# Kernel optimization log

Measured on AMD Instinct MI355X. Metric: run time of the kernel, lower is better.

## Reference

```python
import jax, jax.numpy as jnp
import numpy as np

B, L, D, DIN, S, R, K = 2, 1024, 1024, 2048, 16, 64, 4


def setup_inputs() -> dict:
    key = jax.random.key(0)
    ks = jax.random.split(key, 8)
    f = lambda k, sh, sc: jax.random.normal(k, sh, jnp.float32) * sc
    return {
        "x": f(ks[0], (B, L, D), 1.0),
        "norm_w": jnp.ones((D,), jnp.float32),
        "W_in": f(ks[1], (D, 2 * DIN), D ** -0.5),
        "conv_w": f(ks[2], (DIN, 1, K), 0.5),
        "conv_b": jnp.zeros((DIN,), jnp.float32),
        "W_x": f(ks[3], (DIN, R + 2 * S), DIN ** -0.5),
        "W_dt": f(ks[4], (R, DIN), R ** -0.5),
        "b_dt": f(ks[5], (DIN,), 0.1),
        "A_log": jnp.log(jnp.broadcast_to(jnp.arange(1, S + 1, dtype=jnp.float32), (DIN, S))),
        "D_skip": jnp.ones((DIN,), jnp.float32),
        "W_out": f(ks[6], (DIN, D), DIN ** -0.5),
    }


def reference(x, norm_w, W_in, conv_w, conv_b, W_x, W_dt, b_dt, A_log, D_skip, W_out):
    eps = 1e-5
    # RMSNorm
    xn = x * jax.lax.rsqrt(jnp.mean(x * x, axis=-1, keepdims=True) + eps) * norm_w
    # input projection -> (x_branch, gate)
    xz = xn @ W_in                       # [B,L,2*DIN]
    xi, z = jnp.split(xz, 2, axis=-1)
    # causal depthwise conv1d along L
    xt = jnp.transpose(xi, (0, 2, 1))    # [B,DIN,L]
    xc = jax.lax.conv_general_dilated(xt, conv_w, (1,), [(K - 1, 0)],
                                      feature_group_count=DIN)
    xc = jnp.transpose(xc, (0, 2, 1)) + conv_b
    xc = jax.nn.silu(xc)                 # [B,L,DIN]
    # input-dependent SSM parameters
    xd = xc @ W_x                        # [B,L,R+2S]
    dt, Bm, Cm = jnp.split(xd, [R, R + S], axis=-1)
    dt = jax.nn.softplus(dt @ W_dt + b_dt)           # [B,L,DIN]
    A = -jnp.exp(A_log)                              # [DIN,S]
    dA = jnp.exp(dt[..., None] * A)                  # [B,L,DIN,S]
    dBu = (dt * xc)[..., None] * Bm[:, :, None, :]   # [B,L,DIN,S]
    # selective scan: h_t = dA_t * h_{t-1} + dBu_t (parallel associative scan)
    def comb(c1, c2):
        a1, b1 = c1
        a2, b2 = c2
        return a1 * a2, a2 * b1 + b2
    _, h = jax.lax.associative_scan(comb, (dA, dBu), axis=1)
    y = jnp.einsum('blds,bls->bld', h, Cm) + D_skip * xc
    y = y * jax.nn.silu(z)
    return x + y @ W_out
```

## Files before the change

### kernel.cpp

```cpp
#include <hip/hip_runtime.h>

#define B_    2
#define L_    1024
#define D_    1024
#define DIN_  2048
#define S_    16
#define R_    64
#define NTOK  (B_ * L_)
#define NCH   32
#define LC    (L_ / NCH)

typedef unsigned short u16;
typedef short bf16x8 __attribute__((ext_vector_type(8)));
typedef float f32x4  __attribute__((ext_vector_type(4)));

__device__ __forceinline__ u16 f2bf(float f) {
    union { float f; unsigned u; } v; v.f = f;
    return (u16)((v.u + 0x7FFFu + ((v.u >> 16) & 1u)) >> 16);
}
__device__ __forceinline__ float bf2f(u16 b) {
    union { unsigned u; float f; } v; v.u = (unsigned)b << 16;
    return v.f;
}

__device__ __forceinline__ void transp_tile(
    const float* __restrict__ src, u16* __restrict__ dst,
    int R, int Csrc, int cx, int cy, int tx, int ty) {
    __shared__ float tile[32][33];
    int c0 = cx * 32, r0 = cy * 32;
#pragma unroll
    for (int i = 0; i < 32; i += 8)
        tile[ty + i][tx] = (c0 + tx < Csrc)
            ? src[(size_t)(r0 + ty + i) * Csrc + c0 + tx] : 0.f;
    __syncthreads();
#pragma unroll
    for (int i = 0; i < 32; i += 8)
        dst[(size_t)(c0 + ty + i) * R + r0 + tx] = f2bf(tile[tx][ty + i]);
}

__global__ __launch_bounds__(256) void prep_kernel(
    const float* __restrict__ x, const float* __restrict__ nw, u16* __restrict__ xn,
    const float* __restrict__ W_in,  u16* __restrict__ WinT,
    const float* __restrict__ W_out, u16* __restrict__ WoutT,
    const float* __restrict__ W_x,   u16* __restrict__ WxT,
    const float* __restrict__ W_dt,  u16* __restrict__ WdtT) {
    int bid = blockIdx.x;
    if (bid < NTOK) {
        int row = bid;
        const float4 v = ((const float4*)(x + (size_t)row * D_))[threadIdx.x];
        float ss = v.x * v.x + v.y * v.y + v.z * v.z + v.w * v.w;
#pragma unroll
        for (int o = 32; o > 0; o >>= 1) ss += __shfl_down(ss, o);
        __shared__ float red[4];
        if ((threadIdx.x & 63) == 0) red[threadIdx.x >> 6] = ss;
        __syncthreads();
        float tot = red[0] + red[1] + red[2] + red[3];
        float sc = rsqrtf(tot * (1.f / (float)D_) + 1e-5f);
        const float4 wv = ((const float4*)nw)[threadIdx.x];
        ushort4 o;
        o.x = f2bf(v.x * sc * wv.x);
        o.y = f2bf(v.y * sc * wv.y);
        o.z = f2bf(v.z * sc * wv.z);
        o.w = f2bf(v.w * sc * wv.w);
        ((ushort4*)(xn + (size_t)row * D_))[threadIdx.x] = o;
        return;
    }
    int b2 = bid - NTOK;
    int tx = threadIdx.x & 31, ty = threadIdx.x >> 5;
    if (b2 < 4096) {
        transp_tile(W_in, WinT, D_, 2 * DIN_, b2 % 128, b2 / 128, tx, ty);
    } else if (b2 < 6144) {
        int b = b2 - 4096;
        transp_tile(W_out, WoutT, DIN_, D_, b % 32, b / 32, tx, ty);
    } else if (b2 < 6400) {
        int b = b2 - 6144;
        transp_tile(W_x, WxT, DIN_, 96, b % 4, b / 4, tx, ty);
    } else {
        int b = b2 - 6400;
        transp_tile(W_dt, WdtT, R_, DIN_, b % 64, b / 64, tx, ty);
    }
}

#define BK 32
template<int BM, int BN, int CX>
__global__ __launch_bounds__(512, 8) void gemm_bf16(
    const u16* __restrict__ A, int lda,
    const u16* __restrict__ Bt, int ldb,
    float* __restrict__ C, u16* __restrict__ Cbf, int ldc,
    const float* __restrict__ aux,
    int M, int N, int K, int mode) {
    constexpr int WROWS = BM / 32;
    constexpr int WCOLS = BN / 32;
    static_assert(WROWS * WCOLS == 8, "8 waves");
    constexpr int FM = 2;
    constexpr int FN = 2;
    constexpr int ABYTES = BM * BK * 2;
    constexpr int BBYTES = BN * BK * 2;
    __shared__ __align__(16) u16 As[2][BM * BK];
    __shared__ __align__(16) u16 Bs[2][BN * BK];
    const int t = threadIdx.x;
    const int w = t >> 6;
    const int l = t & 63;
    const int lr = l & 15;
    const int kg = l >> 4;
    const int wm = (w / WCOLS) * 32;
    const int wn = (w % WCOLS) * 32;

    const int GX = gridDim.x, GY = gridDim.y;
    int h = blockIdx.x + GX * (blockIdx.y + GY * blockIdx.z);
    int xcd = h & 7, pos = h >> 3;
    int ncx = GX / CX;
    int chunk = (GX * GY * gridDim.z) >> 3;
    int rpc = chunk / CX;
    int bx = (xcd % ncx) * CX + pos % CX;
    int r  = (xcd / ncx) * rpc + pos / CX;
    int by = r % GY;
    int bz = r / GY;

    const int row0 = by * BM;
    const int col0 = bx * BN;
    const int kbase = bz * K;

    auto stage = [&](int buf, int k0) {
        if (t < ABYTES / 16) {
            int off = t * 16;
            int grow = off >> 6;
            int sw = ((off >> 4) & 3) ^ ((grow >> 1) & 3);
            const u16* ga = A + (size_t)(row0 + grow) * lda + k0 + sw * 8;
            __builtin_amdgcn_global_load_lds(
                (const __attribute__((address_space(1))) unsigned int*)(const void*)ga,
                (__attribute__((address_space(3))) unsigned int*)(void*)&As[buf][off >> 1],
                16, 0, 0);
        }
        if (t < BBYTES / 16) {
            int off = t * 16;
            int grow = off >> 6;
            int sw = ((off >> 4) & 3) ^ ((grow >> 1) & 3);
            const u16* gb = Bt + (size_t)(col0 + grow) * ldb + k0 + sw * 8;
            __builtin_amdgcn_global_load_lds(
                (const __attribute__((address_space(1))) unsigned int*)(const void*)gb,
                (__attribute__((address_space(3))) unsigned int*)(void*)&Bs[buf][off >> 1],
                16, 0, 0);
        }
    };

    f32x4 acc[FM][FN];
#pragma unroll
    for (int i = 0; i < FM; ++i)
#pragma unroll
        for (int j = 0; j < FN; ++j) acc[i][j] = (f32x4){0.f, 0.f, 0.f, 0.f};

    const int nt = K / BK;
    stage(0, kbase);
    asm volatile("s_waitcnt vmcnt(0)" ::: "memory");
    __builtin_amdgcn_s_barrier();
    asm volatile("" ::: "memory");

    int cur = 0;
    for (int tt = 0; tt < nt; ++tt) {
        if (tt + 1 < nt) stage(cur ^ 1, kbase + (tt + 1) * BK);
        bf16x8 af[FM], bfr[FN];
#pragma unroll
        for (int mt = 0; mt < FM; ++mt) {
            int ar = wm + mt * 16 + lr;
            af[mt] = *(const bf16x8*)&As[cur][ar * 32 + (kg ^ ((ar >> 1) & 3)) * 8];
        }
#pragma unroll
        for (int nt2 = 0; nt2 < FN; ++nt2) {
            int br = wn + nt2 * 16 + lr;
            bfr[nt2] = *(const bf16x8*)&Bs[cur][br * 32 + (kg ^ ((br >> 1) & 3)) * 8];
        }
        __builtin_amdgcn_s_setprio(1);
#pragma unroll
        for (int mt = 0; mt < FM; ++mt)
#pragma unroll
            for (int nt2 = 0; nt2 < FN; ++nt2)
                acc[mt][nt2] = __builtin_amdgcn_mfma_f32_16x16x32_bf16(
                    af[mt], bfr[nt2], acc[mt][nt2], 0, 0, 0);
        __builtin_amdgcn_s_setprio(0);
        if (tt + 1 < nt) {
            asm volatile("s_waitcnt vmcnt(0)" ::: "memory");
            __builtin_amdgcn_s_barrier();
            asm volatile("" ::: "memory");
        }
        cur ^= 1;
    }

    size_t pbase = (mode == 3) ? (size_t)bz * M * N : 0;
#pragma unroll
    for (int mt = 0; mt < FM; ++mt) {
#pragma unroll
        for (int nt2 = 0; nt2 < FN; ++nt2) {
#pragma unroll
            for (int r2 = 0; r2 < 4; ++r2) {
                int row = row0 + wm + mt * 16 + kg * 4 + r2;
                int col = col0 + wn + nt2 * 16 + lr;
                float v = acc[mt][nt2][r2];
                if (mode == 1) { v += aux[col]; v = (v > 20.f) ? v : log1pf(__expf(v)); }
                else if (mode == 2) { v += aux[(size_t)row * ldc + col]; }
                if (C)   C[pbase + (size_t)row * ldc + col] = v;
                if (Cbf) Cbf[pbase + (size_t)row * ldc + col] = f2bf(v);
            }
        }
    }
}

__global__ __launch_bounds__(256) void reduce_wx_kernel(
    const u16* __restrict__ part, u16* __restrict__ xdb) {
    int i = blockIdx.x * 256 + threadIdx.x;
    float sx = 0.f, sy = 0.f, sz = 0.f, sw = 0.f;
#pragma unroll
    for (int k = 0; k < 16; ++k) {
        ushort4 v = ((const ushort4*)(part + (size_t)k * NTOK * 128))[i];
        sx += bf2f(v.x); sy += bf2f(v.y); sz += bf2f(v.z); sw += bf2f(v.w);
    }
    ushort4 o; o.x = f2bf(sx); o.y = f2bf(sy); o.z = f2bf(sz); o.w = f2bf(sw);
    ((ushort4*)xdb)[i] = o;
}

__global__ __launch_bounds__(256) void reduce_out_kernel(
    const u16* __restrict__ part, const float* __restrict__ x, float* __restrict__ out) {
    int i = blockIdx.x * 256 + threadIdx.x;
    float sx = 0.f, sy = 0.f, sz = 0.f, sw = 0.f;
#pragma unroll
    for (int k = 0; k < 4; ++k) {
        ushort4 v = ((const ushort4*)(part + (size_t)k * NTOK * D_))[i];
        sx += bf2f(v.x); sy += bf2f(v.y); sz += bf2f(v.z); sw += bf2f(v.w);
    }
    float4 xv = ((const float4*)x)[i];
    float4 s = {sx + xv.x, sy + xv.y, sz + xv.z, sw + xv.w};
    ((float4*)out)[i] = s;
}

__global__ __launch_bounds__(256) void conv_silu_kernel(
    const u16* __restrict__ xzb, const float* __restrict__ cw,
    const float* __restrict__ cb, u16* __restrict__ xcb) {
    size_t idx = (size_t)blockIdx.x * 256 + threadIdx.x;
    int c = (int)(idx & (DIN_ - 1));
    int g = (int)(idx >> 11);
    int bl0 = g * 4;
    int l0 = bl0 & (L_ - 1);
    const float4 w = ((const float4*)cw)[c];
    float bias = cb[c];
    float v[7];
#pragma unroll
    for (int k = 0; k < 7; ++k) {
        int off = k - 3;
        v[k] = (l0 + off >= 0) ? bf2f(xzb[(size_t)(bl0 + off) * 4096 + c]) : 0.f;
    }
#pragma unroll
    for (int j = 0; j < 4; ++j) {
        float acc = bias + v[j] * w.x + v[j + 1] * w.y + v[j + 2] * w.z + v[j + 3] * w.w;
        float s = acc / (1.f + __expf(-acc));
        xcb[(size_t)(bl0 + j) * DIN_ + c] = f2bf(s);
    }
}

__device__ __forceinline__ void load16(const u16* p, float* dst) {
    bf16x8 v0 = *(const bf16x8*)p;
    bf16x8 v1 = *(const bf16x8*)(p + 8);
#pragma unroll
    for (int j = 0; j < 8; ++j) {
        dst[j]     = bf2f((u16)v0[j]);
        dst[8 + j] = bf2f((u16)v1[j]);
    }
}

__global__ __launch_bounds__(256) void scan_chunk_kernel(
    const u16* __restrict__ dtq, const u16* __restrict__ xcb,
    const u16* __restrict__ xdb, const float* __restrict__ A_log,
    u16* __restrict__ Pout, u16* __restrict__ Hout) {
    int din = blockIdx.x * 256 + threadIdx.x;
    int c = blockIdx.y, b = blockIdx.z;
    float a[S_], h[S_];
#pragma unroll
    for (int q = 0; q < 4; ++q) {
        float4 av = ((const float4*)(A_log + (size_t)din * S_))[q];
        a[q * 4 + 0] = -__expf(av.x); a[q * 4 + 1] = -__expf(av.y);
        a[q * 4 + 2] = -__expf(av.z); a[q * 4 + 3] = -__expf(av.w);
    }
#pragma unroll
    for (int s = 0; s < S_; ++s) h[s] = 0.f;
    float sdt = 0.f;
    size_t rbase = (size_t)b * L_ + (size_t)c * LC;
#pragma unroll 2
    for (int i = 0; i < LC; ++i) {
        size_t row = rbase + i;
        float dtv = bf2f(dtq[row * DIN_ + din]);
        float xcv = bf2f(xcb[row * DIN_ + din]);
        float du = dtv * xcv;
        sdt += dtv;
        float Bv[S_];
        load16(xdb + row * 128 + 64, Bv);
#pragma unroll
        for (int s = 0; s < S_; ++s) {
            float dA = __expf(dtv * a[s]);
            h[s] = h[s] * dA + du * Bv[s];
        }
    }
    size_t obase = ((size_t)(b * NCH + c) * DIN_ + din) * S_;
    bf16x8 pv0, pv1, hv0, hv1;
#pragma unroll
    for (int s = 0; s < 8; ++s) {
        pv0[s] = (short)f2bf(__expf(a[s] * sdt));
        pv1[s] = (short)f2bf(__expf(a[8 + s] * sdt));
        hv0[s] = (short)f2bf(h[s]);
        hv1[s] = (short)f2bf(h[8 + s]);
    }
    *(bf16x8*)&Pout[obase] = pv0;
    *(bf16x8*)&Pout[obase + 8] = pv1;
    *(bf16x8*)&Hout[obase] = hv0;
    *(bf16x8*)&Hout[obase + 8] = hv1;
}

__global__ __launch_bounds__(256) void scan_combine_kernel(
    const u16* __restrict__ P, const u16* __restrict__ H,
    float* __restrict__ h0) {
    int tid = blockIdx.x * 256 + threadIdx.x;
    int ds = tid & (DIN_ * S_ - 1);
    int b = tid >> 15;
    float h = 0.f;
#pragma unroll
    for (int c = 0; c < NCH; ++c) {
        size_t idx = ((size_t)(b * NCH + c) * DIN_ * S_) + ds;
        h0[idx] = h;
        h = bf2f(H[idx]) + bf2f(P[idx]) * h;
    }
}

__global__ __launch_bounds__(256) void scan_final_kernel(
    const u16* __restrict__ dtq, const u16* __restrict__ xcb,
    const u16* __restrict__ xdb, const float* __restrict__ A_log,
    const float* __restrict__ h0, const float* __restrict__ Dskip,
    const u16* __restrict__ xzb, u16* __restrict__ yg) {
    int din = blockIdx.x * 256 + threadIdx.x;
    int c = blockIdx.y, b = blockIdx.z;
    float a[S_], h[S_];
#pragma unroll
    for (int q = 0; q < 4; ++q) {
        float4 av = ((const float4*)(A_log + (size_t)din * S_))[q];
        a[q * 4 + 0] = -__expf(av.x); a[q * 4 + 1] = -__expf(av.y);
        a[q * 4 + 2] = -__expf(av.z); a[q * 4 + 3] = -__expf(av.w);
    }
    size_t ibase = ((size_t)(b * NCH + c) * DIN_ + din) * S_;
#pragma unroll
    for (int q = 0; q < 4; ++q) {
        float4 hv = ((const float4*)(h0 + ibase))[q];
        h[q * 4 + 0] = hv.x; h[q * 4 + 1] = hv.y; h[q * 4 + 2] = hv.z; h[q * 4 + 3] = hv.w;
    }
    float dsk = Dskip[din];
    size_t rbase = (size_t)b * L_ + (size_t)c * LC;
#pragma unroll 2
    for (int i = 0; i < LC; ++i) {
        size_t row = rbase + i;
        float dtv = bf2f(dtq[row * DIN_ + din]);
        float xcv = bf2f(xcb[row * DIN_ + din]);
        float du = dtv * xcv;
        float Bv[S_], Cv[S_];
        load16(xdb + row * 128 + 64, Bv);
        load16(xdb + row * 128 + 80, Cv);
        float py = 0.f;
#pragma unroll
        for (int s = 0; s < S_; ++s) {
            float dA = __expf(dtv * a[s]);
            h[s] = h[s] * dA + du * Bv[s];
            py += h[s] * Cv[s];
        }
        float zv = bf2f(xzb[row * 4096 + DIN_ + din]);
        float y = (py + dsk * xcv) * (zv / (1.f + __expf(-zv)));
        yg[row * DIN_ + din] = f2bf(y);
    }
}

extern "C" void kernel_launch(void* const* d_in, const int* in_sizes, int n_in,
                              void* d_out, int out_size, void* d_ws, size_t ws_size,
                              hipStream_t stream) {
    const float* x      = (const float*)d_in[0];
    const float* norm_w = (const float*)d_in[1];
    const float* W_in   = (const float*)d_in[2];
    const float* conv_w = (const float*)d_in[3];
    const float* conv_b = (const float*)d_in[4];
    const float* W_x    = (const float*)d_in[5];
    const float* W_dt   = (const float*)d_in[6];
    const float* b_dt   = (const float*)d_in[7];
    const float* A_log  = (const float*)d_in[8];
    const float* D_skip = (const float*)d_in[9];
    const float* W_out  = (const float*)d_in[10];
    float* out = (float*)d_out;

    char* p = (char*)d_ws;
    auto alloc = [&](size_t bytes) {
        char* r = p;
        p += (bytes + 255) & ~(size_t)255;
        return r;
    };
    u16*   xn      = (u16*)alloc((size_t)NTOK * D_ * 2);
    u16*   WinT    = (u16*)alloc((size_t)2 * DIN_ * D_ * 2);
    u16*   WoutT   = (u16*)alloc((size_t)D_ * DIN_ * 2);
    u16*   WxT     = (u16*)alloc((size_t)128 * DIN_ * 2);
    u16*   WdtT    = (u16*)alloc((size_t)DIN_ * R_ * 2);
    u16*   xzb     = (u16*)alloc((size_t)NTOK * 2 * DIN_ * 2);
    u16*   xcb     = (u16*)alloc((size_t)NTOK * DIN_ * 2);
    u16*   xdb     = (u16*)alloc((size_t)NTOK * 128 * 2);
    u16*   dtq     = (u16*)alloc((size_t)NTOK * DIN_ * 2);
    u16*   yg      = (u16*)alloc((size_t)NTOK * DIN_ * 2);
    u16*   Pbuf    = (u16*)alloc((size_t)B_ * NCH * DIN_ * S_ * 2);
    u16*   Hbuf    = (u16*)alloc((size_t)B_ * NCH * DIN_ * S_ * 2);
    float* h0buf   = (float*)alloc((size_t)B_ * NCH * DIN_ * S_ * 4);
    u16*   part_out = (u16*)alloc((size_t)4 * NTOK * D_ * 2);
    u16*   part_wx  = part_out;

    prep_kernel<<<NTOK + 6528, 256, 0, stream>>>(
        x, norm_w, xn, W_in, WinT, W_out, WoutT, W_x, WxT, W_dt, WdtT);

    gemm_bf16<64, 128, 8><<<dim3(2 * DIN_ / 128, NTOK / 64), 512, 0, stream>>>(
        xn, D_, WinT, D_, nullptr, xzb, 2 * DIN_, nullptr, NTOK, 2 * DIN_, D_, 0);
    conv_silu_kernel<<<(NTOK * DIN_ / 4) / 256, 256, 0, stream>>>(xzb, conv_w, conv_b, xcb);
    gemm_bf16<64, 128, 1><<<dim3(1, NTOK / 64, 16), 512, 0, stream>>>(
        xcb, DIN_, WxT, DIN_, nullptr, part_wx, 128, nullptr, NTOK, 128, DIN_ / 16, 3);
    reduce_wx_kernel<<<(NTOK * 128 / 4) / 256, 256, 0, stream>>>(part_wx, xdb);
    gemm_bf16<64, 128, 8><<<dim3(DIN_ / 128, NTOK / 64), 512, 0, stream>>>(
        xdb, 128, WdtT, R_, nullptr, dtq, DIN_, b_dt, NTOK, DIN_, R_, 1);
    {
        dim3 grid(DIN_ / 256, NCH, B_);
        scan_chunk_kernel<<<grid, 256, 0, stream>>>(dtq, xcb, xdb, A_log, Pbuf, Hbuf);
        scan_combine_kernel<<<(B_ * DIN_ * S_) / 256, 256, 0, stream>>>(Pbuf, Hbuf, h0buf);
        scan_final_kernel<<<grid, 256, 0, stream>>>(dtq, xcb, xdb, A_log, h0buf, D_skip, xzb, yg);
    }
    gemm_bf16<64, 128, 8><<<dim3(D_ / 128, NTOK / 64, 4), 512, 0, stream>>>(
        yg, DIN_, WoutT, DIN_, nullptr, part_out, D_, nullptr, NTOK, D_, DIN_ / 4, 3);
    reduce_out_kernel<<<(NTOK * D_ / 4) / 256, 256, 0, stream>>>(part_out, x, out);
}
```

Measured before the change: 155.9 us.

## Fuse three-phase chunked scan into one cooperative kernel with grid syncs

Merges the scan chunk, combine and final kernels into a single cooperative launch that separates the phases with grid-wide syncs and thread fences. It keeps the A coefficients and chunk indices in registers across phases and removes two kernel launches and their launch gaps. In exchange, every block (512 here) must be co-resident, and the combine phase now runs on only 64K threads inside the larger grid. Grid sync overhead and the register pressure of keeping state live across phases may offset the gain.

```diff
diff --git a/kernel.cpp b/kernel.cpp
--- a/kernel.cpp
+++ b/kernel.cpp
@@ -1,4 +1,7 @@
 #include <hip/hip_runtime.h>
+#include <hip/hip_cooperative_groups.h>
+
+namespace cg = cooperative_groups;
 
 #define B_    2
 #define L_    1024
@@ -266,12 +269,16 @@
     }
 }
 
-__global__ __launch_bounds__(256) void scan_chunk_kernel(
+__global__ __launch_bounds__(256) void scan_coop_kernel(
     const u16* __restrict__ dtq, const u16* __restrict__ xcb,
     const u16* __restrict__ xdb, const float* __restrict__ A_log,
-    u16* __restrict__ Pout, u16* __restrict__ Hout) {
-    int din = blockIdx.x * 256 + threadIdx.x;
-    int c = blockIdx.y, b = blockIdx.z;
+    u16* __restrict__ Pbuf, u16* __restrict__ Hbuf, float* __restrict__ h0,
+    const float* __restrict__ Dskip, const u16* __restrict__ xzb,
+    u16* __restrict__ yg) {
+    cg::grid_group grid = cg::this_grid();
+    const int din = blockIdx.x * 256 + threadIdx.x;
+    const int c = blockIdx.y, b = blockIdx.z;
+
     float a[S_], h[S_];
 #pragma unroll
     for (int q = 0; q < 4; ++q) {
@@ -283,6 +290,7 @@
     for (int s = 0; s < S_; ++s) h[s] = 0.f;
     float sdt = 0.f;
     size_t rbase = (size_t)b * L_ + (size_t)c * LC;
+
 #pragma unroll 2
     for (int i = 0; i < LC; ++i) {
         size_t row = rbase + i;
@@ -299,57 +307,47 @@
         }
     }
     size_t obase = ((size_t)(b * NCH + c) * DIN_ + din) * S_;
-    bf16x8 pv0, pv1, hv0, hv1;
-#pragma unroll
-    for (int s = 0; s < 8; ++s) {
-        pv0[s] = (short)f2bf(__expf(a[s] * sdt));
-        pv1[s] = (short)f2bf(__expf(a[8 + s] * sdt));
-        hv0[s] = (short)f2bf(h[s]);
-        hv1[s] = (short)f2bf(h[8 + s]);
-    }
-    *(bf16x8*)&Pout[obase] = pv0;
-    *(bf16x8*)&Pout[obase + 8] = pv1;
-    *(bf16x8*)&Hout[obase] = hv0;
-    *(bf16x8*)&Hout[obase + 8] = hv1;
-}
-
-__global__ __launch_bounds__(256) void scan_combine_kernel(
-    const u16* __restrict__ P, const u16* __restrict__ H,
-    float* __restrict__ h0) {
-    int tid = blockIdx.x * 256 + threadIdx.x;
-    int ds = tid & (DIN_ * S_ - 1);
-    int b = tid >> 15;
-    float h = 0.f;
-#pragma unroll
-    for (int c = 0; c < NCH; ++c) {
-        size_t idx = ((size_t)(b * NCH + c) * DIN_ * S_) + ds;
-        h0[idx] = h;
-        h = bf2f(H[idx]) + bf2f(P[idx]) * h;
-    }
-}
-
-__global__ __launch_bounds__(256) void scan_final_kernel(
-    const u16* __restrict__ dtq, const u16* __restrict__ xcb,
-    const u16* __restrict__ xdb, const float* __restrict__ A_log,
-    const float* __restrict__ h0, const float* __restrict__ Dskip,
-    const u16* __restrict__ xzb, u16* __restrict__ yg) {
-    int din = blockIdx.x * 256 + threadIdx.x;
-    int c = blockIdx.y, b = blockIdx.z;
-    float a[S_], h[S_];
+    {
+        bf16x8 pv0, pv1, hv0, hv1;
+#pragma unroll
+        for (int s = 0; s < 8; ++s) {
+            pv0[s] = (short)f2bf(__expf(a[s] * sdt));
+            pv1[s] = (short)f2bf(__expf(a[8 + s] * sdt));
+            hv0[s] = (short)f2bf(h[s]);
+            hv1[s] = (short)f2bf(h[8 + s]);
+        }
+        *(bf16x8*)&Pbuf[obase] = pv0;
+        *(bf16x8*)&Pbuf[obase + 8] = pv1;
+        *(bf16x8*)&Hbuf[obase] = hv0;
+        *(bf16x8*)&Hbuf[obase + 8] = hv1;
+    }
+    __threadfence();
+    grid.sync();
+
+    {
+        int bid = blockIdx.x + gridDim.x * (blockIdx.y + gridDim.y * blockIdx.z);
+        int gtid = bid * 256 + threadIdx.x;
+        if (gtid < B_ * DIN_ * S_) {
+            int ds = gtid & (DIN_ * S_ - 1);
+            int b2 = gtid >> 15;
+            float hh = 0.f;
+#pragma unroll
+            for (int cc = 0; cc < NCH; ++cc) {
+                size_t idx = ((size_t)(b2 * NCH + cc) * DIN_ * S_) + ds;
+                h0[idx] = hh;
+                hh = bf2f(Hbuf[idx]) + bf2f(Pbuf[idx]) * hh;
+            }
+        }
+    }
+    __threadfence();
+    grid.sync();
+
 #pragma unroll
     for (int q = 0; q < 4; ++q) {
-        float4 av = ((const float4*)(A_log + (size_t)din * S_))[q];
-        a[q * 4 + 0] = -__expf(av.x); a[q * 4 + 1] = -__expf(av.y);
-        a[q * 4 + 2] = -__expf(av.z); a[q * 4 + 3] = -__expf(av.w);
-    }
-    size_t ibase = ((size_t)(b * NCH + c) * DIN_ + din) * S_;
-#pragma unroll
-    for (int q = 0; q < 4; ++q) {
-        float4 hv = ((const float4*)(h0 + ibase))[q];
+        float4 hv = ((const float4*)(h0 + obase))[q];
         h[q * 4 + 0] = hv.x; h[q * 4 + 1] = hv.y; h[q * 4 + 2] = hv.z; h[q * 4 + 3] = hv.w;
     }
     float dsk = Dskip[din];
-    size_t rbase = (size_t)b * L_ + (size_t)c * LC;
 #pragma unroll 2
     for (int i = 0; i < LC; ++i) {
         size_t row = rbase + i;
@@ -398,7 +396,7 @@
     u16*   WinT    = (u16*)alloc((size_t)2 * DIN_ * D_ * 2);
     u16*   WoutT   = (u16*)alloc((size_t)D_ * DIN_ * 2);
     u16*   WxT     = (u16*)alloc((size_t)128 * DIN_ * 2);
-    u16*   WdtT    = (u16*)alloc((size_t)DIN_ * R_ * 2);
+    u16*   WdtT   = (u16*)alloc((size_t)DIN_ * R_ * 2);
     u16*   xzb     = (u16*)alloc((size_t)NTOK * 2 * DIN_ * 2);
     u16*   xcb     = (u16*)alloc((size_t)NTOK * DIN_ * 2);
     u16*   xdb     = (u16*)alloc((size_t)NTOK * 128 * 2);
@@ -422,10 +420,14 @@
     gemm_bf16<64, 128, 8><<<dim3(DIN_ / 128, NTOK / 64), 512, 0, stream>>>(
         xdb, 128, WdtT, R_, nullptr, dtq, DIN_, b_dt, NTOK, DIN_, R_, 1);
     {
-        dim3 grid(DIN_ / 256, NCH, B_);
-        scan_chunk_kernel<<<grid, 256, 0, stream>>>(dtq, xcb, xdb, A_log, Pbuf, Hbuf);
-        scan_combine_kernel<<<(B_ * DIN_ * S_) / 256, 256, 0, stream>>>(Pbuf, Hbuf, h0buf);
-        scan_final_kernel<<<grid, 256, 0, stream>>>(dtq, xcb, xdb, A_log, h0buf, D_skip, xzb, yg);
+        void* kargs[] = {
+            (void*)&dtq, (void*)&xcb, (void*)&xdb, (void*)&A_log,
+            (void*)&Pbuf, (void*)&Hbuf, (void*)&h0buf,
+            (void*)&D_skip, (void*)&xzb, (void*)&yg
+        };
+        hipLaunchCooperativeKernel((void*)scan_coop_kernel,
+                                   dim3(DIN_ / 256, NCH, B_), dim3(256),
+                                   kargs, 0, stream);
     }
     gemm_bf16<64, 128, 8><<<dim3(D_ / 128, NTOK / 64, 4), 512, 0, stream>>>(
         yg, DIN_, WoutT, DIN_, nullptr, part_out, D_, nullptr, NTOK, D_, DIN_ / 4, 3);
```

After: 392.5 us. +151.8%, slower.
